# Kernel tuning notes

Measured on AMD Instinct MI355X. Metric: run time of the kernel, lower is better.

## Reference

```python
import jax, jax.numpy as jnp
import numpy as np


def setup_inputs() -> dict:
    key = jax.random.key(0)
    k1, k2, k3 = jax.random.split(key, 3)
    B, N, D = 16, 512, 256
    # integer frame durations per token, 4..11 frames (avg ~7.5)
    durations = jax.random.randint(k1, (B, N), 4, 12, dtype=jnp.int32)
    # T = max over batch of total frames (static python int, mirrors torch.arange(0, max(s)))
    total_len = int(jnp.max(jnp.sum(durations, axis=-1)))
    x = jax.random.normal(k2, (B, N, D), dtype=jnp.float32)
    # positive Gaussian range (std) per token
    ranges = jax.random.uniform(k3, (B, N), minval=0.5, maxval=4.0, dtype=jnp.float32)
    return {"x": x, "durations": durations, "ranges": ranges, "total_len": total_len}


def _gaussian_weights(durations, ranges, total_len):
    # e: cumulative end frame per token, c: Gaussian center per token
    e = jnp.cumsum(durations, axis=-1).astype(jnp.float32)          # [B, N]
    c = (e - 0.5 * durations.astype(jnp.float32))[..., None]        # [B, N, 1]
    t = jnp.arange(total_len, dtype=jnp.float32)[None, None, :]     # [1, 1, T]
    inv_r2 = ranges[..., None] ** (-2)                               # [B, N, 1]
    w1 = jnp.exp(-inv_r2 * (t - c) ** 2)                             # [B, N, T]
    # original computes the exp twice (w_1 and inside w_2); same math, computed once
    w2 = jnp.sum(w1, axis=1, keepdims=True) + 1e-20                  # [B, 1, T]
    return w1 / w2


def _create_positions(durations, total_len):
    # frame-index-within-token positions: pos[b, t] = t - start_of_segment(t)
    e = jnp.cumsum(durations, axis=-1)                               # [B, N]
    starts = e - durations                                           # [B, N]
    t = jnp.arange(total_len, dtype=durations.dtype)                 # [T]
    seg = jax.vmap(lambda eb: jnp.searchsorted(eb, t, side='right'))(e)  # [B, T]
    seg = jnp.clip(seg, 0, durations.shape[-1] - 1)
    return t[None, :] - jnp.take_along_axis(starts, seg, axis=-1)    # [B, T]


def reference(x, durations, ranges, total_len):
    weights = _gaussian_weights(durations, ranges, total_len)        # [B, N, T]
    # matmul(weights.transpose(1,2), x) -> [B, T, D]
    out = jnp.einsum('bnt,bnd->btd', weights, x)
    positions = _create_positions(durations, total_len)
    return positions, out, weights
```

## Files before the change

### kernel.cpp

```cpp
#include <hip/hip_runtime.h>
#include <hip/hip_bf16.h>


#define TT  64
#define NWC 44
#define WBS 72
#define MARGIN 42.0f
#define RPB 8

typedef __attribute__((ext_vector_type(8))) short short8;
typedef __attribute__((ext_vector_type(8))) unsigned short ushort8;
typedef __attribute__((ext_vector_type(4))) float f32x4;

__device__ inline unsigned short f2bf(float f) {
    union { float f; unsigned int u; } v; v.f = f;
    unsigned int u = v.u;
    return (unsigned short)((u + 0x7FFFu + ((u >> 16) & 1u)) >> 16);
}

__global__ void scan_kernel(const int* __restrict__ dur,
                            const float* __restrict__ ranges,
                            float* __restrict__ c, float* __restrict__ ir,
                            int* __restrict__ e_i, int* __restrict__ st_i) {
    const int N = 512;
    int b = blockIdx.x, tid = threadIdx.x;
    __shared__ int sc[512];
    int d = dur[b * N + tid];
    sc[tid] = d;
    __syncthreads();
    for (int off = 1; off < 512; off <<= 1) {
        int add = (tid >= off) ? sc[tid - off] : 0;
        __syncthreads();
        sc[tid] += add;
        __syncthreads();
    }
    int e = sc[tid];
    float r = ranges[b * N + tid];
    c[b * N + tid]    = (float)e - 0.5f * (float)d;
    ir[b * N + tid]   = 1.0f / (r * r);
    e_i[b * N + tid]  = e;
    st_i[b * N + tid] = e - d;
}

__global__ __launch_bounds__(256) void pass1_kernel(
        const float* __restrict__ x, const float* __restrict__ c,
        const float* __restrict__ ir,
        const int* __restrict__ e_i, const int* __restrict__ st_i,
        float* __restrict__ pos_out ,
        float* __restrict__ out1 ,
        float* __restrict__ iw2_ws ,
        int T) {
    const int N = 512, D = 256;
    int b = blockIdx.y;
    int t0 = blockIdx.x * TT;
    int tid = threadIdx.x;

    __shared__ float c_s[512];
    __shared__ float ir_s[512];
    __shared__ int   es[512], ss[512];
    __shared__ __align__(16) unsigned short wb[TT][WBS];
    __shared__ float part[4][TT];
    __shared__ float iw2_s[TT];
    __shared__ int lohi[2];

    for (int i = tid; i < 512; i += 256) {
        c_s[i]  = c[b * N + i];
        ir_s[i] = ir[b * N + i];
        es[i]   = e_i[b * N + i];
        ss[i]   = st_i[b * N + i];
    }
    __syncthreads();

    if (tid == 0) {
        float lo_v = (float)t0 - MARGIN;
        float hi_v = (float)(t0 + TT - 1) + MARGIN;
        int lo = 0, hi = 512;
        while (lo < hi) { int m = (lo + hi) >> 1; if (c_s[m] < lo_v) lo = m + 1; else hi = m; }
        int l = lo;
        lo = 0; hi = 512;
        while (lo < hi) { int m = (lo + hi) >> 1; if (c_s[m] <= hi_v) lo = m + 1; else hi = m; }
        int h = lo - 1;
        if (h > l + NWC - 1) h = l + NWC - 1;
        lohi[0] = l; lohi[1] = h;
    }
    if (tid < TT) {
        int t = t0 + tid;
        if (t < T) {
            int lo = 0, hi = 512;
            while (lo < hi) { int m = (lo + hi) >> 1; if (es[m] <= t) lo = m + 1; else hi = m; }
            int seg = min(lo, 511);
            pos_out[b * T + t] = (float)(t - ss[seg]);
        }
    }
    __syncthreads();
    int lo_u = lohi[0], hi_u = lohi[1];

    int tl = tid & 63;
    int s  = tid >> 6;
    int t  = t0 + tl;

    float p = 0.f;
    #pragma unroll
    for (int jj = 0; jj < 16; jj++) {
        int i = s + 4 * jj;
        int n = lo_u + i;
        float w1 = 0.f;
        if (n <= hi_u && t < T) {
            float d = (float)t - c_s[n];
            w1 = expf(-ir_s[n] * d * d);
        }
        wb[tl][i] = f2bf(w1);
        p += w1;
    }
    part[s][tl] = p;
    __syncthreads();
    if (tid < TT) {
        float w2 = part[0][tid] + part[1][tid] + part[2][tid] + part[3][tid];
        float iw2 = 1.0f / (w2 + 1e-20f);
        iw2_s[tid] = iw2;
        int t2 = t0 + tid;
        if (t2 < T) iw2_ws[b * T + t2] = iw2;
    }
    __syncthreads();

    int lane = tid & 63;
    int l15  = lane & 15;
    int q    = lane >> 4;

    f32x4 acc[16];
    #pragma unroll
    for (int nt = 0; nt < 16; nt++) acc[nt] = (f32x4){0.f, 0.f, 0.f, 0.f};

    const float* xb = x + (size_t)b * N * D;
    #pragma unroll
    for (int ks = 0; ks < 2; ks++) {
        short8 afrag = *(const short8*)&wb[16 * s + l15][ks * 32 + q * 8];
        const float* rp[8];
        #pragma unroll
        for (int j = 0; j < 8; j++) {
            int tok = lo_u + ks * 32 + q * 8 + j;
            tok = min(tok, 511);
            rp[j] = xb + (size_t)tok * D;
        }
        #pragma unroll
        for (int nt = 0; nt < 16; nt++) {
            int d = nt * 16 + l15;
            ushort8 bu;
            #pragma unroll
            for (int j = 0; j < 8; j++) bu[j] = f2bf(rp[j][d]);
            short8 bfrag = (short8)bu;
            acc[nt] = __builtin_amdgcn_mfma_f32_16x16x32_bf16(afrag, bfrag, acc[nt], 0, 0, 0);
        }
    }

    #pragma unroll
    for (int r = 0; r < 4; r++) {
        int tt = t0 + 16 * s + q * 4 + r;
        if (tt < T) {
            float iw2 = iw2_s[16 * s + q * 4 + r];
            float* orow = out1 + ((size_t)b * T + tt) * D;
            #pragma unroll
            for (int nt = 0; nt < 16; nt++)
                orow[nt * 16 + l15] = acc[nt][r] * iw2;
        }
    }
}

__global__ __launch_bounds__(256) void weights_kernel(
        const float* __restrict__ c, const float* __restrict__ ir,
        const float* __restrict__ iw2_ws,
        float* __restrict__ out2 , int T) {
    const int N = 512;
    int b = blockIdx.y;
    int n0 = blockIdx.x * RPB;
    int tid = threadIdx.x;

    for (int r = 0; r < RPB; r++) {
        int n = n0 + r;
        float cn  = c[b * N + n];
        float irn = ir[b * N + n];
        float rad = 10.3f * __frsqrt_rn(irn) + 1.0f;
        int lo = (int)(cn - rad); if (lo < 0) lo = 0;
        int hi = (int)(cn + rad) + 1; if (hi > T) hi = T;

        size_t base = ((size_t)b * N + n) * (size_t)T;
        int head = (int)((4 - (base & 3)) & 3);
        if (head > T) head = T;
        if (tid < head) {
            int t = tid;
            float w = 0.f;
            if (t >= lo && t < hi) {
                float d = (float)t - cn;
                w = expf(-irn * d * d) * iw2_ws[b * T + t];
            }
            out2[base + t] = w;
        }
        int ngrp = (T - head) >> 2;
        int tail = (T - head) & 3;
        float* rowp = (float*)(out2 + base + head);
        for (int g = tid; g < ngrp; g += 256) {
            int tg = head + 4 * g;
            f32x4 v = (f32x4){0.f, 0.f, 0.f, 0.f};
            if (tg + 3 >= lo && tg < hi) {
                #pragma unroll
                for (int k = 0; k < 4; k++) {
                    int t = tg + k;
                    if (t >= lo && t < hi) {
                        float d = (float)t - cn;
                        v[k] = expf(-irn * d * d) * iw2_ws[b * T + t];
                    }
                }
            }
            *(f32x4*)(rowp + 4 * g) = v;
        }
        if (tid < tail) {
            int t = head + 4 * ngrp + tid;
            float w = 0.f;
            if (t >= lo && t < hi) {
                float d = (float)t - cn;
                w = expf(-irn * d * d) * iw2_ws[b * T + t];
            }
            out2[base + t] = w;
        }
    }
}

extern "C" void kernel_launch(void* const* d_in, const int* in_sizes, int n_in,
                              void* d_out, int out_size, void* d_ws, size_t ws_size,
                              hipStream_t stream) {
    const float* x      = (const float*)d_in[0];
    const int*   dur    = (const int*)d_in[1];
    const float* ranges = (const float*)d_in[2];
    const int B = 16, N = 512, D = 256;
    const int T = out_size / (B * (1 + D + N));

    float* pos_out = (float*)d_out;
    float* out1    = pos_out + (size_t)B * T;
    float* out2    = out1 + (size_t)B * T * D;

    float* c      = (float*)d_ws;
    float* ir     = c + B * N;
    int*   e_i    = (int*)(ir + B * N);
    int*   st_i   = e_i + B * N;
    float* iw2_ws = (float*)(st_i + B * N);

    scan_kernel<<<B, 512, 0, stream>>>(dur, ranges, c, ir, e_i, st_i);

    dim3 g1((T + TT - 1) / TT, B);
    pass1_kernel<<<g1, 256, 0, stream>>>(x, c, ir, e_i, st_i, pos_out, out1, iw2_ws, T);

    dim3 g2(N / RPB, B);
    weights_kernel<<<g2, 256, 0, stream>>>(c, ir, iw2_ws, out2, T);
}
```

Baseline: 223.6 us.

## Split pass1 MFMA work by D columns per wave instead of T rows

Each wave in pass1 now computes all 64 time rows for its own 64-column slice of D, rather than 16 rows across all 256 columns. The x operand is therefore loaded and converted to bf16 once per block instead of four times, with the A fragments read from shared memory reused across the N tiles. The weights kernel's rows-per-block is halved to launch more blocks. The accumulator layout changes from 16 to 4x4 tiles per wave, and the output stores become column-sliced per wave.

```diff
diff --git a/kernel.cpp b/kernel.cpp
--- a/kernel.cpp
+++ b/kernel.cpp
@@ -6,7 +6,7 @@
 #define NWC 44
 #define WBS 72
 #define MARGIN 42.0f
-#define RPB 8
+#define RPB 4
 
 typedef __attribute__((ext_vector_type(8))) short short8;
 typedef __attribute__((ext_vector_type(8))) unsigned short ushort8;
@@ -127,14 +127,16 @@
     int l15  = lane & 15;
     int q    = lane >> 4;
 
-    f32x4 acc[16];
-    #pragma unroll
-    for (int nt = 0; nt < 16; nt++) acc[nt] = (f32x4){0.f, 0.f, 0.f, 0.f};
+    f32x4 acc[4][4];
+    #pragma unroll
+    for (int mt = 0; mt < 4; mt++)
+        #pragma unroll
+        for (int nt = 0; nt < 4; nt++)
+            acc[mt][nt] = (f32x4){0.f, 0.f, 0.f, 0.f};
 
     const float* xb = x + (size_t)b * N * D;
     #pragma unroll
     for (int ks = 0; ks < 2; ks++) {
-        short8 afrag = *(const short8*)&wb[16 * s + l15][ks * 32 + q * 8];
         const float* rp[8];
         #pragma unroll
         for (int j = 0; j < 8; j++) {
@@ -142,26 +144,35 @@
             tok = min(tok, 511);
             rp[j] = xb + (size_t)tok * D;
         }
-        #pragma unroll
-        for (int nt = 0; nt < 16; nt++) {
-            int d = nt * 16 + l15;
+        short8 afrag[4];
+        #pragma unroll
+        for (int mt = 0; mt < 4; mt++)
+            afrag[mt] = *(const short8*)&wb[16 * mt + l15][ks * 32 + q * 8];
+        #pragma unroll
+        for (int nt = 0; nt < 4; nt++) {
+            int d = 64 * s + nt * 16 + l15;
             ushort8 bu;
             #pragma unroll
             for (int j = 0; j < 8; j++) bu[j] = f2bf(rp[j][d]);
             short8 bfrag = (short8)bu;
-            acc[nt] = __builtin_amdgcn_mfma_f32_16x16x32_bf16(afrag, bfrag, acc[nt], 0, 0, 0);
-        }
-    }
-
-    #pragma unroll
-    for (int r = 0; r < 4; r++) {
-        int tt = t0 + 16 * s + q * 4 + r;
-        if (tt < T) {
-            float iw2 = iw2_s[16 * s + q * 4 + r];
-            float* orow = out1 + ((size_t)b * T + tt) * D;
             #pragma unroll
-            for (int nt = 0; nt < 16; nt++)
-                orow[nt * 16 + l15] = acc[nt][r] * iw2;
+            for (int mt = 0; mt < 4; mt++)
+                acc[mt][nt] = __builtin_amdgcn_mfma_f32_16x16x32_bf16(afrag[mt], bfrag, acc[mt][nt], 0, 0, 0);
+        }
+    }
+
+    #pragma unroll
+    for (int mt = 0; mt < 4; mt++) {
+        #pragma unroll
+        for (int r = 0; r < 4; r++) {
+            int tt = t0 + 16 * mt + q * 4 + r;
+            if (tt < T) {
+                float iw2 = iw2_s[16 * mt + q * 4 + r];
+                float* orow = out1 + ((size_t)b * T + tt) * D + 64 * s;
+                #pragma unroll
+                for (int nt = 0; nt < 4; nt++)
+                    orow[nt * 16 + l15] = acc[mt][nt][r] * iw2;
+            }
         }
     }
 }
@@ -174,6 +185,7 @@
     int b = blockIdx.y;
     int n0 = blockIdx.x * RPB;
     int tid = threadIdx.x;
+    const f32x4 z4 = (f32x4){0.f, 0.f, 0.f, 0.f};
 
     for (int r = 0; r < RPB; r++) {
         int n = n0 + r;
@@ -200,7 +212,7 @@
         float* rowp = (float*)(out2 + base + head);
         for (int g = tid; g < ngrp; g += 256) {
             int tg = head + 4 * g;
-            f32x4 v = (f32x4){0.f, 0.f, 0.f, 0.f};
+            f32x4 v = z4;
             if (tg + 3 >= lo && tg < hi) {
                 #pragma unroll
                 for (int k = 0; k < 4; k++) {
```

Result: no change. 219.9 us (median of 2 runs) (-1.6%).
